# Optimization experiments

Hardware: AMD Instinct MI355X
Metric: run time of the kernel (lower is better)

The kernel has to match this reference:

```python
import jax, jax.numpy as jnp
import numpy as np
import math

B, L, D, H, FF = 8, 1024, 1024, 16, 4096
DT = D // H  # d_tensor per head
EPS = 1e-12


def _layernorm(x, gamma, beta):
    # Faithful: unbiased std (ddof=1), divide by (std + eps)
    mean = jnp.mean(x, axis=-1, keepdims=True)
    std = jnp.std(x, axis=-1, keepdims=True, ddof=1)
    return gamma * ((x - mean) / (std + EPS)) + beta


def setup_inputs() -> dict:
    key = jax.random.key(0)
    ks = jax.random.split(key, 16)
    sc = 1.0 / math.sqrt(D)
    inp = {
        "x": jax.random.normal(ks[0], (B, L, D), jnp.float32),
        "s_mask": jnp.ones((B, 1, L, L), jnp.int32),
        "wq": jax.random.normal(ks[1], (D, D), jnp.float32) * sc,
        "bq": jnp.zeros((D,), jnp.float32),
        "wk": jax.random.normal(ks[2], (D, D), jnp.float32) * sc,
        "bk": jnp.zeros((D,), jnp.float32),
        "wv": jax.random.normal(ks[3], (D, D), jnp.float32) * sc,
        "bv": jnp.zeros((D,), jnp.float32),
        "wc": jax.random.normal(ks[4], (D, D), jnp.float32) * sc,
        "bc": jnp.zeros((D,), jnp.float32),
        "g1": jnp.ones((D,), jnp.float32),
        "be1": jnp.zeros((D,), jnp.float32),
        "w1": jax.random.normal(ks[5], (D, FF), jnp.float32) * sc,
        "b1": jnp.zeros((FF,), jnp.float32),
        "w2": jax.random.normal(ks[6], (FF, D), jnp.float32) / math.sqrt(FF),
        "b2": jnp.zeros((D,), jnp.float32),
        "g2": jnp.ones((D,), jnp.float32),
        "be2": jnp.zeros((D,), jnp.float32),
    }
    return inp


def reference(x, s_mask, wq, bq, wk, bk, wv, bv, wc, bc, g1, be1, w1, b1, w2, b2, g2, be2):
    _x = x
    q = x @ wq + bq
    k = x @ wk + bk
    v = x @ wv + bv
    # Faithful quirk: split() is a VIEW/reshape [B,L,D] -> [B,H,L,DT], not a transpose-based head split.
    q = q.reshape(B, H, L, DT)
    k = k.reshape(B, H, L, DT)
    v = v.reshape(B, H, L, DT)
    # Faithful quirk: k_t is a reshape to [B,H,DT,L], not a transpose.
    k_t = k.reshape(B, H, DT, L)
    score = jnp.einsum('bhld,bhdm->bhlm', q, k_t) / math.sqrt(DT)
    # Faithful quirk: masked_fill value is -1e-12 (not -inf)
    score = jnp.where(s_mask == 0, jnp.float32(-EPS), score)
    # Faithful quirk: nn.Softmax() with dim=None on 4D tensor -> softmax over dim=1 (head axis)
    score = jax.nn.softmax(score, axis=1)
    out = jnp.einsum('bhlm,bhmd->bhld', score, v)
    out = out.reshape(B, L, D)
    out = out @ wc + bc
    x = _layernorm(out + _x, g1, be1)
    # dropout1: identity at inference
    _x = x
    h = jax.nn.relu(x @ w1 + b1)  # FFN dropout also identity at inference
    h = h @ w2 + b2
    x = _layernorm(h + _x, g2, be2)
    return x
```

## Files before the change

kernel.cpp:

```cpp
#include <hip/hip_runtime.h>
#include <stdint.h>

typedef unsigned short u16;
typedef __attribute__((ext_vector_type(8))) short sx8;
typedef __attribute__((ext_vector_type(4))) float fx4;

__device__ __forceinline__ float bf2f(u16 u) {
    union { unsigned i; float f; } v; v.i = ((unsigned)u) << 16; return v.f;
}
__device__ __forceinline__ u16 f2bf(float f) {
    union { float f; unsigned i; } v; v.f = f;
    return (u16)((v.i + 0x7FFFu + ((v.i >> 16) & 1u)) >> 16);
}
#define MFMA(a, b, c) __builtin_amdgcn_mfma_f32_16x16x32_bf16((a), (b), (c), 0, 0, 0)

#define GLDS(gp, lp) \
    __builtin_amdgcn_global_load_lds((const __attribute__((address_space(1))) void*)(gp), \
                                     (__attribute__((address_space(3))) void*)(lp), 16, 0, 0)

#define QSCALE 0.18033688011112042f
#define MASKC (-1.442695e-12f)

template<int BN>
__global__ __launch_bounds__(256) void gemm_bt(
    const u16* __restrict__ A, long sA, int ldA,
    const u16* __restrict__ BT, long sBT, int ldBT,
    u16* __restrict__ C, long sC, int ldC,
    int K,
    const u16* __restrict__ bias, int bz,
    const void* __restrict__ resid, int residF32, long rofs,
    float scale, int scaleZ0, int relu)
{
    constexpr int BK = 32;
    constexpr int TM = 4;
    constexpr int TN = BN / 32;
    constexpr int AI = 2;
    constexpr int BI = BN / 64;

    __shared__ __align__(16) u16 As[128 * BK];
    __shared__ __align__(16) u16 Bs[BN * BK];

    const int tid  = threadIdx.x;
    const int w    = tid >> 6;
    const int lane = tid & 63;
    const int quad = lane >> 4;
    const int n16  = lane & 15;
    const int wrow = w >> 1, wcol = w & 1;

    int bx = blockIdx.x, by = blockIdx.y;
    {
        int nxy = gridDim.x * gridDim.y;
        if ((nxy & 7) == 0) {
            int bid = by * gridDim.x + bx;
            int wgs = (bid & 7) * (nxy >> 3) + (bid >> 3);
            bx = wgs % gridDim.x;
            by = wgs / gridDim.x;
        }
    }
    const int m0 = by * 128, n0 = bx * BN;
    const long z = blockIdx.z;
    const float es = (z == 0 || !scaleZ0) ? scale : 1.f;
    A  += z * sA;
    BT += z * sBT;
    C  += z * sC;

    fx4 acc[TM][TN] = {};

    for (int k0 = 0; k0 < K; k0 += BK) {
        #pragma unroll
        for (int i = 0; i < AI; ++i) {
            unsigned base = (unsigned)(w * AI + i) * 1024u;
            unsigned off  = base + (unsigned)lane * 16u;
            unsigned row  = off >> 6;
            unsigned col  = (off & 63u) >> 1;
            GLDS(A + (long)(m0 + row) * ldA + k0 + col, (char*)As + base);
        }
        #pragma unroll
        for (int i = 0; i < BI; ++i) {
            unsigned base = (unsigned)(w * BI + i) * 1024u;
            unsigned off  = base + (unsigned)lane * 16u;
            unsigned row  = off >> 6;
            unsigned col  = (off & 63u) >> 1;
            GLDS(BT + (long)(n0 + row) * ldBT + k0 + col, (char*)Bs + base);
        }
        __syncthreads();

        sx8 af[TM], bfr[TN];
        #pragma unroll
        for (int r = 0; r < TM; ++r)
            af[r] = *(const sx8*)&As[(wrow * 64 + r * 16 + n16) * BK + quad * 8];
        #pragma unroll
        for (int c = 0; c < TN; ++c)
            bfr[c] = *(const sx8*)&Bs[(wcol * (TN * 16) + c * 16 + n16) * BK + quad * 8];
        #pragma unroll
        for (int r = 0; r < TM; ++r)
            #pragma unroll
            for (int c = 0; c < TN; ++c)
                acc[r][c] = MFMA(af[r], bfr[c], acc[r][c]);
        __syncthreads();
    }

    #pragma unroll
    for (int r = 0; r < TM; ++r) {
        int row = m0 + wrow * 64 + r * 16 + quad * 4;
        #pragma unroll
        for (int c = 0; c < TN; ++c) {
            int col = n0 + wcol * (TN * 16) + c * 16 + n16;
            float bv = bias ? bf2f(bias[bz * (int)z + col]) : 0.f;
            #pragma unroll
            for (int g = 0; g < 4; ++g) {
                long idx = (long)(row + g) * ldC + col;
                float xv = acc[r][c][g] * es + bv;
                if (resid)
                    xv += residF32 ? ((const float*)resid)[rofs + idx]
                                   : bf2f(((const u16*)resid)[rofs + idx]);
                if (relu) xv = fmaxf(xv, 0.f);
                C[idx] = f2bf(xv);
            }
        }
    }
}

__global__ __launch_bounds__(256, 2) void attn_fused(
    const u16* __restrict__ qb, const u16* __restrict__ kt,
    const u16* __restrict__ vt, const int* __restrict__ mask,
    u16* __restrict__ p0, u16* __restrict__ p1)
{
    constexpr int MC = 64;
    constexpr int LM = MC + 8;
    constexpr int SH = 16 * LM;
    __shared__ __align__(16) u16 Ss[2][16 * SH];

    const int tid = threadIdx.x, w = tid >> 6, lane = tid & 63;
    const int quad = lane >> 4, n16 = lane & 15;

    const int wg = ((blockIdx.x & 7) << 7) + (blockIdx.x >> 3);
    const int l0 = (wg & 63) * 16;
    const long bo = (long)((wg >> 6) & 7) * 1048576;
    const int zz = wg >> 9;
    const int mbase = zz * 512;
    u16* __restrict__ po = zz ? p1 : p0;

    const int sl0 = tid >> 5,         smp0 = (tid & 31) * 2;
    const int sl1 = (tid + 256) >> 5, smp1 = ((tid + 256) & 31) * 2;

    sx8 qf[4][2];
    #pragma unroll
    for (int i = 0; i < 4; ++i) {
        const u16* qp = qb + bo + (w * 4 + i) * 65536 + (l0 + n16) * 64 + quad * 8;
        qf[i][0] = *(const sx8*)qp;
        qf[i][1] = *(const sx8*)(qp + 32);
    }

    fx4 of[4][4] = {};

    auto do_qk = [&](int t, u16* S) {
        const int m0 = mbase + t * MC;
        #pragma unroll
        for (int i = 0; i < 4; ++i) {
            const int h = w * 4 + i;
            const u16* kp = kt + bo + h * 65536 + (long)m0 * 64;
            #pragma unroll
            for (int nt = 0; nt < 4; ++nt) {
                const u16* kr = kp + (nt * 16 + n16) * 64 + quad * 8;
                fx4 s = {};
                s = MFMA(*(const sx8*)kr,        qf[i][0], s);
                s = MFMA(*(const sx8*)(kr + 32), qf[i][1], s);
                uint2 pk;
                pk.x = (unsigned)f2bf(s[0]) | ((unsigned)f2bf(s[1]) << 16);
                pk.y = (unsigned)f2bf(s[2]) | ((unsigned)f2bf(s[3]) << 16);
                *(uint2*)&S[h * SH + n16 * LM + nt * 16 + quad * 4] = pk;
            }
        }
    };

    auto do_softmax = [&](int t, u16* S) {
        const int m0 = mbase + t * MC;
        const int2 mk0 = *(const int2*)&mask[bo + (long)(l0 + sl0) * 1024 + m0 + smp0];
        const int2 mk1 = *(const int2*)&mask[bo + (long)(l0 + sl1) * 1024 + m0 + smp1];
        #pragma unroll
        for (int j = 0; j < 2; ++j) {
            const int l = j ? sl1 : sl0, mp = j ? smp1 : smp0;
            const int2 mk = j ? mk1 : mk0;
            u16* col = &S[l * LM + mp];
            float v0[16], v1[16], mx0 = -1e30f, mx1 = -1e30f;
            #pragma unroll
            for (int h = 0; h < 16; ++h) {
                unsigned pr = *(const unsigned*)&col[h * SH];
                float a = (mk.x == 0) ? MASKC : bf2f((u16)(pr & 0xffff));
                float b = (mk.y == 0) ? MASKC : bf2f((u16)(pr >> 16));
                v0[h] = a; v1[h] = b;
                mx0 = fmaxf(mx0, a); mx1 = fmaxf(mx1, b);
            }
            float s0 = 0.f, s1 = 0.f;
            #pragma unroll
            for (int h = 0; h < 16; ++h) {
                v0[h] = exp2f(v0[h] - mx0); s0 += v0[h];
                v1[h] = exp2f(v1[h] - mx1); s1 += v1[h];
            }
            const float i0 = __builtin_amdgcn_rcpf(s0);
            const float i1 = __builtin_amdgcn_rcpf(s1);
            #pragma unroll
            for (int h = 0; h < 16; ++h) {
                float e0 = v0[h] * i0, e1 = v1[h] * i1;
                unsigned pk_;
                asm("v_cvt_pk_bf16_f32 %0, %1, %2" : "=v"(pk_) : "v"(e0), "v"(e1));
                *(unsigned*)&col[h * SH] = pk_;
            }
        }
    };

    auto do_pv = [&](int t, const u16* S) {
        const int m0 = mbase + t * MC;
        #pragma unroll
        for (int i = 0; i < 4; ++i) {
            const int h = w * 4 + i;
            const u16* sp = &S[h * SH + n16 * LM];
            sx8 a0 = *(const sx8*)(sp + quad * 8);
            sx8 a1 = *(const sx8*)(sp + 32 + quad * 8);
            const u16* vp = vt + bo + h * 65536 + (long)n16 * 1024 + m0 + quad * 8;
            #pragma unroll
            for (int dt = 0; dt < 4; ++dt) {
                of[i][dt] = MFMA(a0, *(const sx8*)(vp + dt * 16384),      of[i][dt]);
                of[i][dt] = MFMA(a1, *(const sx8*)(vp + dt * 16384 + 32), of[i][dt]);
            }
        }
    };

    do_qk(0, Ss[0]);
    __syncthreads();
    for (int it = 0; it < 8; ++it) {
        const int cur = it & 1;
        if (it < 7) do_qk(it + 1, Ss[cur ^ 1]);
        do_softmax(it, Ss[cur]);
        __syncthreads();
        do_pv(it, Ss[cur]);
        __syncthreads();
    }

    #pragma unroll
    for (int i = 0; i < 4; ++i) {
        const int h = w * 4 + i;
        #pragma unroll
        for (int dt = 0; dt < 4; ++dt)
            #pragma unroll
            for (int r = 0; r < 4; ++r)
                po[bo + h * 65536 + (long)(l0 + quad * 4 + r) * 64 + dt * 16 + n16]
                    = f2bf(of[i][dt][r]);
    }
}

__global__ __launch_bounds__(256) void add_bf(
    const u16* __restrict__ a, u16* __restrict__ b)
{
    long i = ((long)blockIdx.x * 256 + threadIdx.x) * 8;
    uint4 x = *(const uint4*)(a + i);
    uint4 y = *(const uint4*)(b + i);
    uint4 r;
    unsigned* xp = (unsigned*)&x; unsigned* yp = (unsigned*)&y; unsigned* rp = (unsigned*)&r;
    #pragma unroll
    for (int k = 0; k < 4; ++k) {
        float lo = bf2f((u16)(xp[k] & 0xffff)) + bf2f((u16)(yp[k] & 0xffff));
        float hi = bf2f((u16)(xp[k] >> 16))    + bf2f((u16)(yp[k] >> 16));
        rp[k] = (unsigned)f2bf(lo) | ((unsigned)f2bf(hi) << 16);
    }
    *(uint4*)(b + i) = r;
}

__global__ __launch_bounds__(256) void convert_f2b(
    const float* __restrict__ in, u16* __restrict__ out)
{
    long i = ((long)blockIdx.x * 256 + threadIdx.x) * 4;
    fx4 v = *(const fx4*)(in + i);
    uint2 o;
    o.x = (unsigned)f2bf(v[0]) | ((unsigned)f2bf(v[1]) << 16);
    o.y = (unsigned)f2bf(v[2]) | ((unsigned)f2bf(v[3]) << 16);
    *(uint2*)(out + i) = o;
}

__global__ __launch_bounds__(256) void transpose4_f2b(
    const float* a0, const float* a1, const float* a2, const float* a3,
    u16* __restrict__ out)
{
    __shared__ float t[32][33];
    const float* in = blockIdx.z == 0 ? a0 : blockIdx.z == 1 ? a1
                    : blockIdx.z == 2 ? a2 : a3;
    out += (long)blockIdx.z * 1048576;
    int c0 = blockIdx.x * 32, r0 = blockIdx.y * 32;
    int tx = threadIdx.x & 31, ty = threadIdx.x >> 5;
    #pragma unroll
    for (int i = 0; i < 4; ++i)
        t[ty + i * 8][tx] = in[(long)(r0 + ty + i * 8) * 1024 + c0 + tx];
    __syncthreads();
    #pragma unroll
    for (int i = 0; i < 4; ++i)
        out[(long)(c0 + ty + i * 8) * 1024 + r0 + tx] = f2bf(t[tx][ty + i * 8]);
}

__global__ __launch_bounds__(256) void transpose_f2b(
    const float* __restrict__ in, u16* __restrict__ out, int R, int C)
{
    __shared__ float t[32][33];
    int c0 = blockIdx.x * 32, r0 = blockIdx.y * 32;
    int tx = threadIdx.x & 31, ty = threadIdx.x >> 5;
    #pragma unroll
    for (int i = 0; i < 4; ++i)
        t[ty + i * 8][tx] = in[(long)(r0 + ty + i * 8) * C + c0 + tx];
    __syncthreads();
    #pragma unroll
    for (int i = 0; i < 4; ++i)
        out[(long)(c0 + ty + i * 8) * R + r0 + tx] = f2bf(t[tx][ty + i * 8]);
}

__global__ __launch_bounds__(256) void transpose_bf(
    const u16* __restrict__ in, u16* __restrict__ out, int R, int C)
{
    __shared__ u16 t[32][33];
    long zoff = (long)blockIdx.z * (long)R * (long)C;
    in += zoff; out += zoff;
    int c0 = blockIdx.x * 32, r0 = blockIdx.y * 32;
    int tx = threadIdx.x & 31, ty = threadIdx.x >> 5;
    #pragma unroll
    for (int i = 0; i < 4; ++i)
        t[ty + i * 8][tx] = in[(long)(r0 + ty + i * 8) * C + c0 + tx];
    __syncthreads();
    #pragma unroll
    for (int i = 0; i < 4; ++i)
        out[(long)(c0 + ty + i * 8) * R + r0 + tx] = t[tx][ty + i * 8];
}

__global__ __launch_bounds__(256) void pack_bias(
    const float* bq, const float* bk, const float* bv, const float* bc,
    const float* b1, const float* b2, u16* __restrict__ out)
{
    int i = blockIdx.x * 256 + threadIdx.x;
    float v;
    if      (i < 1024) v = bq[i] * QSCALE;
    else if (i < 2048) v = bk[i - 1024];
    else if (i < 3072) v = bv[i - 2048];
    else if (i < 4096) v = bc[i - 3072];
    else if (i < 8192) v = b1[i - 4096];
    else               v = b2[i - 8192];
    out[i] = f2bf(v);
}

__global__ __launch_bounds__(256) void layernorm_row(
    const u16* __restrict__ in, const float* __restrict__ g,
    const float* __restrict__ be, void* __restrict__ out, int outF32)
{
    int wave = threadIdx.x >> 6, lane = threadIdx.x & 63;
    long row = (long)blockIdx.x * 4 + wave;
    const u16* p = in + row * 1024 + lane * 16;

    float x[16];
    uint4 a = ((const uint4*)p)[0], b = ((const uint4*)p)[1];
    {
        unsigned u;
        u = a.x; x[0] = bf2f(u & 0xffff);  x[1] = bf2f(u >> 16);
        u = a.y; x[2] = bf2f(u & 0xffff);  x[3] = bf2f(u >> 16);
        u = a.z; x[4] = bf2f(u & 0xffff);  x[5] = bf2f(u >> 16);
        u = a.w; x[6] = bf2f(u & 0xffff);  x[7] = bf2f(u >> 16);
        u = b.x; x[8] = bf2f(u & 0xffff);  x[9] = bf2f(u >> 16);
        u = b.y; x[10] = bf2f(u & 0xffff); x[11] = bf2f(u >> 16);
        u = b.z; x[12] = bf2f(u & 0xffff); x[13] = bf2f(u >> 16);
        u = b.w; x[14] = bf2f(u & 0xffff); x[15] = bf2f(u >> 16);
    }
    float s = 0.f, ss = 0.f;
    #pragma unroll
    for (int i = 0; i < 16; ++i) { s += x[i]; ss += x[i] * x[i]; }
    #pragma unroll
    for (int o = 32; o >= 1; o >>= 1) { s += __shfl_down(s, o); ss += __shfl_down(ss, o); }
    s = __shfl(s, 0); ss = __shfl(ss, 0);
    float mean = s * (1.f / 1024.f);
    float var  = fmaxf((ss - 1024.f * mean * mean) * (1.f / 1023.f), 0.f);
    float rinv = 1.f / (sqrtf(var) + 1e-12f);

    int col = lane * 16;
    if (outF32) {
        float* ov = (float*)out + row * 1024 + col;
        #pragma unroll
        for (int i = 0; i < 16; ++i)
            ov[i] = g[col + i] * ((x[i] - mean) * rinv) + be[col + i];
    } else {
        u16* ov = (u16*)out + row * 1024 + col;
        #pragma unroll
        for (int i = 0; i < 16; ++i)
            ov[i] = f2bf(g[col + i] * ((x[i] - mean) * rinv) + be[col + i]);
    }
}

extern "C" void kernel_launch(void* const* d_in, const int* in_sizes, int n_in,
                              void* d_out, int out_size, void* d_ws, size_t ws_size,
                              hipStream_t stream)
{
    const float* xf  = (const float*)d_in[0];
    const int* mask  = (const int*)d_in[1];
    const float* wq = (const float*)d_in[2];  const float* bq = (const float*)d_in[3];
    const float* wk = (const float*)d_in[4];  const float* bk = (const float*)d_in[5];
    const float* wv = (const float*)d_in[6];  const float* bv = (const float*)d_in[7];
    const float* wc = (const float*)d_in[8];  const float* bc = (const float*)d_in[9];
    const float* g1 = (const float*)d_in[10]; const float* be1 = (const float*)d_in[11];
    const float* w1 = (const float*)d_in[12]; const float* b1 = (const float*)d_in[13];
    const float* w2 = (const float*)d_in[14]; const float* b2 = (const float*)d_in[15];
    const float* g2 = (const float*)d_in[16]; const float* be2 = (const float*)d_in[17];

    char* ws = (char*)d_ws;
    const long MB = 1 << 20;
    u16* xb    = (u16*)(ws + 0 * MB);
    u16* wqkvT = (u16*)(ws + 16 * MB);
    u16* wcT   = (u16*)(ws + 22 * MB);
    u16* qb    = (u16*)(ws + 24 * MB);
    u16* kb    = (u16*)(ws + 40 * MB);
    u16* vb    = (u16*)(ws + 56 * MB);
    u16* kt    = (u16*)(ws + 72 * MB);
    u16* vt    = (u16*)(ws + 40 * MB);
    u16* biasp = (u16*)(ws + 96 * MB);
    u16* p0   = xb;
    u16* p1   = vb;
    u16* ao   = p1;
    u16* t0   = qb;
    u16* fh   = kb;
    u16* w1T  = (u16*)(ws + 72 * MB);
    u16* w2T  = (u16*)(ws + 80 * MB);
    u16* pre2 = (u16*)(ws + 88 * MB);

    dim3 blk(256);
    const long M1 = 1048576;

    convert_f2b<<<dim3(8192), blk, 0, stream>>>(xf, xb);
    transpose4_f2b<<<dim3(32, 32, 4), blk, 0, stream>>>(wq, wk, wv, wc, wqkvT);
    pack_bias<<<dim3(36), blk, 0, stream>>>(bq, bk, bv, bc, b1, b2, biasp);

    gemm_bt<128><<<dim3(8, 64, 3), blk, 0, stream>>>(
        xb, 0, 1024, wqkvT, M1, 1024, qb, 8 * M1, 1024, 1024,
        biasp, 1024, nullptr, 0, 0, QSCALE, 1, 0);

    transpose_bf<<<dim3(32, 2, 128), blk, 0, stream>>>(kb, kt, 64, 1024);

    transpose_bf<<<dim3(2, 32, 128), blk, 0, stream>>>(vb, vt, 1024, 64);
    attn_fused<<<dim3(1024), blk, 0, stream>>>(qb, kt, vt, mask, p0, p1);
    add_bf<<<dim3(4096), blk, 0, stream>>>(p0, p1);

    gemm_bt<128><<<dim3(8, 64, 1), blk, 0, stream>>>(
        ao, 0, 1024, wcT, 0, 1024, t0, 0, 1024, 1024,
        biasp + 3072, 0, xf, 1, 0, 1.f, 0, 0);
    layernorm_row<<<dim3(2048), blk, 0, stream>>>(t0, g1, be1, t0, 0);

    transpose_f2b<<<dim3(128, 32), blk, 0, stream>>>(w1, w1T, 1024, 4096);
    transpose_f2b<<<dim3(32, 128), blk, 0, stream>>>(w2, w2T, 4096, 1024);

    for (int c = 0; c < 2; ++c) {
        long r0 = (long)c * 4096 * 1024;
        gemm_bt<128><<<dim3(32, 32, 1), blk, 0, stream>>>(
            t0 + r0, 0, 1024, w1T, 0, 1024, fh, 0, 4096, 1024,
            biasp + 4096, 0, nullptr, 0, 0, 1.f, 0, 1);
        gemm_bt<64><<<dim3(16, 32, 1), blk, 0, stream>>>(
            fh, 0, 4096, w2T, 0, 4096, pre2, 0, 1024, 4096,
            biasp + 8192, 0, t0 + r0, 0, 0, 1.f, 0, 0);
        layernorm_row<<<dim3(1024), blk, 0, stream>>>(
            pre2, g2, be2, (float*)d_out + r0, 1);
    }
}
```

Measured before the change: 900.8 us.

## Triple-buffer attention score tiles with a three-stage QK/softmax/PV pipeline

Halves the key-chunk width in the fused attention kernel from 64 to 32 and replaces the double buffer with three rotating LDS buffers. Each iteration now computes QK for chunk t+2, softmax for chunk t+1 and PV for chunk t, with one barrier per iteration instead of two. The goal is to cut synchronisation stalls and overlap MFMA work with the softmax VALU work. In exchange the loop runs twice as many iterations with smaller MFMA batches per step, and LDS use grows from two buffers to three smaller ones.

```diff
diff --git a/kernel.cpp b/kernel.cpp
--- a/kernel.cpp
+++ b/kernel.cpp
@@ -126,10 +126,11 @@
     const u16* __restrict__ vt, const int* __restrict__ mask,
     u16* __restrict__ p0, u16* __restrict__ p1)
 {
-    constexpr int MC = 64;
+    constexpr int MC = 32;
     constexpr int LM = MC + 8;
     constexpr int SH = 16 * LM;
-    __shared__ __align__(16) u16 Ss[2][16 * SH];
+    constexpr int NB = 16 * SH;
+    __shared__ __align__(16) u16 Ss[3 * NB];
 
     const int tid = threadIdx.x, w = tid >> 6, lane = tid & 63;
     const int quad = lane >> 4, n16 = lane & 15;
@@ -141,8 +142,7 @@
     const int mbase = zz * 512;
     u16* __restrict__ po = zz ? p1 : p0;
 
-    const int sl0 = tid >> 5,         smp0 = (tid & 31) * 2;
-    const int sl1 = (tid + 256) >> 5, smp1 = ((tid + 256) & 31) * 2;
+    const int sl = tid >> 4, smp = (tid & 15) * 2;
 
     sx8 qf[4][2];
     #pragma unroll
@@ -161,7 +161,7 @@
             const int h = w * 4 + i;
             const u16* kp = kt + bo + h * 65536 + (long)m0 * 64;
             #pragma unroll
-            for (int nt = 0; nt < 4; ++nt) {
+            for (int nt = 0; nt < 2; ++nt) {
                 const u16* kr = kp + (nt * 16 + n16) * 64 + quad * 8;
                 fx4 s = {};
                 s = MFMA(*(const sx8*)kr,        qf[i][0], s);
@@ -176,37 +176,31 @@
 
     auto do_softmax = [&](int t, u16* S) {
         const int m0 = mbase + t * MC;
-        const int2 mk0 = *(const int2*)&mask[bo + (long)(l0 + sl0) * 1024 + m0 + smp0];
-        const int2 mk1 = *(const int2*)&mask[bo + (long)(l0 + sl1) * 1024 + m0 + smp1];
-        #pragma unroll
-        for (int j = 0; j < 2; ++j) {
-            const int l = j ? sl1 : sl0, mp = j ? smp1 : smp0;
-            const int2 mk = j ? mk1 : mk0;
-            u16* col = &S[l * LM + mp];
-            float v0[16], v1[16], mx0 = -1e30f, mx1 = -1e30f;
-            #pragma unroll
-            for (int h = 0; h < 16; ++h) {
-                unsigned pr = *(const unsigned*)&col[h * SH];
-                float a = (mk.x == 0) ? MASKC : bf2f((u16)(pr & 0xffff));
-                float b = (mk.y == 0) ? MASKC : bf2f((u16)(pr >> 16));
-                v0[h] = a; v1[h] = b;
-                mx0 = fmaxf(mx0, a); mx1 = fmaxf(mx1, b);
-            }
-            float s0 = 0.f, s1 = 0.f;
-            #pragma unroll
-            for (int h = 0; h < 16; ++h) {
-                v0[h] = exp2f(v0[h] - mx0); s0 += v0[h];
-                v1[h] = exp2f(v1[h] - mx1); s1 += v1[h];
-            }
-            const float i0 = __builtin_amdgcn_rcpf(s0);
-            const float i1 = __builtin_amdgcn_rcpf(s1);
-            #pragma unroll
-            for (int h = 0; h < 16; ++h) {
-                float e0 = v0[h] * i0, e1 = v1[h] * i1;
-                unsigned pk_;
-                asm("v_cvt_pk_bf16_f32 %0, %1, %2" : "=v"(pk_) : "v"(e0), "v"(e1));
-                *(unsigned*)&col[h * SH] = pk_;
-            }
+        const int2 mk = *(const int2*)&mask[bo + (long)(l0 + sl) * 1024 + m0 + smp];
+        u16* col = &S[sl * LM + smp];
+        float v0[16], v1[16], mx0 = -1e30f, mx1 = -1e30f;
+        #pragma unroll
+        for (int h = 0; h < 16; ++h) {
+            unsigned pr = *(const unsigned*)&col[h * SH];
+            float a = (mk.x == 0) ? MASKC : bf2f((u16)(pr & 0xffff));
+            float b = (mk.y == 0) ? MASKC : bf2f((u16)(pr >> 16));
+            v0[h] = a; v1[h] = b;
+            mx0 = fmaxf(mx0, a); mx1 = fmaxf(mx1, b);
+        }
+        float s0 = 0.f, s1 = 0.f;
+        #pragma unroll
+        for (int h = 0; h < 16; ++h) {
+            v0[h] = exp2f(v0[h] - mx0); s0 += v0[h];
+            v1[h] = exp2f(v1[h] - mx1); s1 += v1[h];
+        }
+        const float i0 = __builtin_amdgcn_rcpf(s0);
+        const float i1 = __builtin_amdgcn_rcpf(s1);
+        #pragma unroll
+        for (int h = 0; h < 16; ++h) {
+            float e0 = v0[h] * i0, e1 = v1[h] * i1;
+            unsigned pk_;
+            asm("v_cvt_pk_bf16_f32 %0, %1, %2" : "=v"(pk_) : "v"(e0), "v"(e1));
+            *(unsigned*)&col[h * SH] = pk_;
         }
     };
 
@@ -215,27 +209,28 @@
         #pragma unroll
         for (int i = 0; i < 4; ++i) {
             const int h = w * 4 + i;
-            const u16* sp = &S[h * SH + n16 * LM];
-            sx8 a0 = *(const sx8*)(sp + quad * 8);
-            sx8 a1 = *(const sx8*)(sp + 32 + quad * 8);
+            sx8 af = *(const sx8*)&S[h * SH + n16 * LM + quad * 8];
             const u16* vp = vt + bo + h * 65536 + (long)n16 * 1024 + m0 + quad * 8;
             #pragma unroll
-            for (int dt = 0; dt < 4; ++dt) {
-                of[i][dt] = MFMA(a0, *(const sx8*)(vp + dt * 16384),      of[i][dt]);
-                of[i][dt] = MFMA(a1, *(const sx8*)(vp + dt * 16384 + 32), of[i][dt]);
-            }
+            for (int dt = 0; dt < 4; ++dt)
+                of[i][dt] = MFMA(af, *(const sx8*)(vp + dt * 16384), of[i][dt]);
         }
     };
 
-    do_qk(0, Ss[0]);
+    u16* bA = Ss;
+    u16* bB = Ss + NB;
+    u16* bC = Ss + 2 * NB;
+    do_qk(0, bA);
     __syncthreads();
-    for (int it = 0; it < 8; ++it) {
-        const int cur = it & 1;
-        if (it < 7) do_qk(it + 1, Ss[cur ^ 1]);
-        do_softmax(it, Ss[cur]);
+    do_qk(1, bB);
+    do_softmax(0, bA);
+    __syncthreads();
+    for (int t = 0; t < 16; ++t) {
+        if (t + 2 < 16) do_qk(t + 2, bC);
+        if (t + 1 < 16) do_softmax(t + 1, bB);
+        do_pv(t, bA);
         __syncthreads();
-        do_pv(it, Ss[cur]);
-        __syncthreads();
+        u16* tmp = bA; bA = bB; bB = bC; bC = tmp;
     }
 
     #pragma unroll
```

Result: no change. 900.0 us (-0.1%).
